# Optimization experiments

Hardware: AMD Instinct MI355X
Metric: run time of the kernel (lower is better)

The kernel has to match this reference:

```python
import jax, jax.numpy as jnp
import numpy as np

MIN_VAL = 0.0
MAX_VAL = 1.0
NUM_BINS = 512
NUM_NODES = 128
GRAD_SMOOTH = 0.01
BIN_W = (MAX_VAL - MIN_VAL) / NUM_BINS


def _make_kernels():
    sobel = jnp.array([-1.0, 0.0, 1.0], dtype=jnp.float32) / (2.0 * BIN_W)
    r = max(1, int(GRAD_SMOOTH / BIN_W))  # kernel radius in bins
    idx = jnp.arange(2 * r + 1, dtype=jnp.float32) - r
    sigma = GRAD_SMOOTH / BIN_W
    g = jnp.exp(-0.5 * (idx / sigma) ** 2)
    return sobel, g / jnp.sum(g)


def _conv1d_reflect(x, k):
    # x: [N, B], k: [K]; torch Conv1d = cross-correlation with reflect padding
    pad = (k.shape[0] - 1) // 2
    xp = jnp.pad(x, ((0, 0), (pad, pad)), mode='reflect')
    out = jax.lax.conv_general_dilated(
        xp[:, None, :], k[None, None, :], (1,), 'VALID',
        dimension_numbers=('NCH', 'OIH', 'NCH'))
    return out[:, 0, :]


def _compute_cdf_pdf(residuals, weights, src_indices, dst_indices):
    # histogram bin per sample (floor)
    bi = jnp.floor((residuals - MIN_VAL) / BIN_W).astype(jnp.int32)
    valid = (bi >= 0) & (bi < NUM_BINS)
    bi = jnp.clip(bi, 0, NUM_BINS - 1)
    wc = (weights * valid).reshape(-1)  # [N_pairs*K]

    src_comb = (src_indices[:, None] * NUM_BINS + bi).reshape(-1)
    dst_comb = (dst_indices[:, None] * NUM_BINS + bi).reshape(-1)
    nseg = NUM_NODES * NUM_BINS
    hist = (jax.ops.segment_sum(wc, src_comb, num_segments=nseg)
            + jax.ops.segment_sum(wc, dst_comb, num_segments=nseg))
    hist = hist.reshape(NUM_NODES, NUM_BINS)

    wflat = weights.reshape(-1)
    src_exp = jnp.broadcast_to(src_indices[:, None], residuals.shape).reshape(-1)
    dst_exp = jnp.broadcast_to(dst_indices[:, None], residuals.shape).reshape(-1)
    tw = (jax.ops.segment_sum(wflat, src_exp, num_segments=NUM_NODES)
          + jax.ops.segment_sum(wflat, dst_exp, num_segments=NUM_NODES))

    pmf = hist / (tw[:, None] + 1e-10)
    cdf = jnp.cumsum(pmf, axis=1)
    sobel, gauss = _make_kernels()
    pdf = _conv1d_reflect(_conv1d_reflect(cdf, sobel), gauss)
    return cdf, pdf


def _lookup(residuals, weights, cdf, pdf, src_indices, dst_indices):
    # rounded bin for lookup (floor of x + 0.5)
    bi = jnp.floor((residuals - MIN_VAL) / BIN_W + 0.5).astype(jnp.int32)
    valid = (bi >= 0) & (bi < NUM_BINS) & (weights > 0.0)
    bi = jnp.clip(bi, 0, NUM_BINS - 1)
    src_cdf = cdf[src_indices[:, None], bi]
    dst_cdf = cdf[dst_indices[:, None], bi]
    src_grad = pdf[src_indices[:, None], bi] * weights
    dst_grad = pdf[dst_indices[:, None], bi] * weights
    two = jnp.float32(2.0)
    return (jnp.where(valid, src_cdf, two),
            jnp.where(valid, src_grad, 0.0),
            jnp.where(valid, dst_cdf, two),
            jnp.where(valid, dst_grad, 0.0))


def setup_inputs() -> dict:
    key = jax.random.key(0)
    k1, k2, k3, k4 = jax.random.split(key, 4)
    N_pairs, K = 1024, 16384
    return {
        'residuals': jax.random.uniform(k1, (N_pairs, K), dtype=jnp.float32),
        'weights': jax.random.uniform(k2, (N_pairs, K), dtype=jnp.float32),
        'src_indices': jax.random.randint(k3, (N_pairs,), 0, NUM_NODES),
        'dst_indices': jax.random.randint(k4, (N_pairs,), 0, NUM_NODES),
    }


def reference(residuals, weights, src_indices, dst_indices):
    cdf, pdf = _compute_cdf_pdf(residuals, weights, src_indices, dst_indices)
    src_cdf, _, dst_cdf, _ = _lookup(residuals, weights, cdf, pdf,
                                     src_indices, dst_indices)
    return src_cdf, dst_cdf
```

## Files before the change

### kernel.cpp

```cpp
#include <hip/hip_runtime.h>

#define NUM_BINS  512
#define NUM_NODES 128
#define K_ELEMS   16384
#define N_PAIRS   1024
#define NCOPY     16

typedef float f32x4 __attribute__((ext_vector_type(4)));
typedef float f32x2 __attribute__((ext_vector_type(2)));
typedef unsigned int   u32;
typedef unsigned short u16;

__device__ __forceinline__ void gfadd(float* p, float v) { unsafeAtomicAdd(p, v); }

__global__ __launch_bounds__(256) void zero_ws_kernel(float* __restrict__ ws, int n)
{
    int i = blockIdx.x * 256 + threadIdx.x;
    if (i < n) ws[i] = 0.0f;
}

__global__ __launch_bounds__(512) void hist_kernel(
    const float* __restrict__ residuals, const float* __restrict__ weights,
    const int* __restrict__ src, const int* __restrict__ dst,
    float* __restrict__ hist, float* __restrict__ tw,
    u32* __restrict__ mask)
{
    __shared__ u32 lh[NUM_BINS * NCOPY];
    __shared__ float swsum[8];
    const int row  = blockIdx.x;
    const int t    = threadIdx.x;
    const int copy = t & 15;

    uint4* lh4 = (uint4*)lh;
    #pragma unroll
    for (int k = 0; k < NUM_BINS * NCOPY / 4 / 512; ++k) {
        uint4 z; z.x = z.y = z.z = z.w = 0u;
        lh4[t + k * 512] = z;
    }
    __syncthreads();

    const f32x4* r4 = (const f32x4*)(residuals + (size_t)row * K_ELEMS);
    const f32x4* w4 = (const f32x4*)(weights   + (size_t)row * K_ELEMS);

    float wsum = 0.0f;
    u32 vbits = 0;

    f32x4 rA = r4[t];
    f32x4 wA = __builtin_nontemporal_load(w4 + t);
    #pragma unroll
    for (int it = 0; it < K_ELEMS / 4 / 512; ++it) {
        f32x4 rB, wB;
        if (it < K_ELEMS / 4 / 512 - 1) {
            rB = r4[t + (it + 1) * 512];
            wB = __builtin_nontemporal_load(w4 + (t + (it + 1) * 512));
        }
        wsum += wA[0] + wA[1] + wA[2] + wA[3];
        #pragma unroll
        for (int c = 0; c < 4; ++c) {
            int b = (int)floorf(rA[c] * 512.0f);
            if ((unsigned)b < 512u)
                atomicAdd(&lh[b * NCOPY + copy], (u32)fmaf(wA[c], 65536.0f, 0.5f));
            int lb = (int)floorf(rA[c] * 512.0f + 0.5f);
            if (((unsigned)lb < 512u) & (wA[c] > 0.0f))
                vbits |= 1u << (it * 4 + c);
        }
        rA = rB; wA = wB;
    }
    mask[(size_t)row * 512 + t] = vbits;

    #pragma unroll
    for (int off = 32; off > 0; off >>= 1) wsum += __shfl_down(wsum, off, 64);
    const int wave = t >> 6, lane = t & 63;
    if (lane == 0) swsum[wave] = wsum;
    __syncthreads();

    const int s = src[row], d = dst[row];
    if (t == 0) {
        float tot = 0.0f;
        #pragma unroll
        for (int i = 0; i < 8; ++i) tot += swsum[i];
        gfadd(&tw[s], tot);
        gfadd(&tw[d], tot);
    }

    {
        u32 tot = 0;
        #pragma unroll
        for (int cc = 0; cc < NCOPY; ++cc)
            tot += lh[t * NCOPY + ((t + cc) & 15)];
        float v = (float)tot * (1.0f / 65536.0f);
        gfadd(&hist[s * NUM_BINS + t], v);
        gfadd(&hist[d * NUM_BINS + t], v);
    }
}

__global__ __launch_bounds__(512) void lookup_scan_kernel(
    const float* __restrict__ residuals, const u32* __restrict__ mask,
    const int* __restrict__ src, const int* __restrict__ dst,
    const float* __restrict__ hist, const float* __restrict__ tw,
    float* __restrict__ out_src, float* __restrict__ out_dst)
{
    __shared__ f32x2 sd[NUM_BINS];
    const int row = blockIdx.x;
    const int t   = threadIdx.x;

    const size_t base = (size_t)row * K_ELEMS;
    const f32x4* r4   = (const f32x4*)(residuals + base);

    f32x4 rr0 = r4[t],           rr1 = r4[t + 512];
    f32x4 rr2 = r4[t + 1024],    rr3 = r4[t + 1536];
    f32x4 rr4 = r4[t + 2048],    rr5 = r4[t + 2560];
    f32x4 rr6 = r4[t + 3072],    rr7 = r4[t + 3584];
    const u32 mw = mask[(size_t)row * 512 + t];

    const int s = src[row], d = dst[row];
    {
        f32x2 v;
        v[0] = hist[s * NUM_BINS + t] / (tw[s] + 1e-10f);
        v[1] = hist[d * NUM_BINS + t] / (tw[d] + 1e-10f);
        sd[t] = v;
    }
    __syncthreads();

    for (int off = 1; off < NUM_BINS; off <<= 1) {
        f32x2 add = (t >= off) ? sd[t - off] : (f32x2){0.0f, 0.0f};
        __syncthreads();
        sd[t] += add;
        __syncthreads();
    }

    f32x4* os4 = (f32x4*)(out_src + base);
    f32x4* od4 = (f32x4*)(out_dst + base);

    #define EMIT(IT, RV)                                                       \
    {                                                                          \
        f32x4 osv, odv;                                                        \
        _Pragma("unroll")                                                      \
        for (int c = 0; c < 4; ++c) {                                          \
            int lb = (int)floorf(RV[c] * 512.0f + 0.5f);                       \
            int bc = min(max(lb, 0), NUM_BINS - 1);                            \
            bool v = (mw >> (IT * 4 + c)) & 1u;                                \
            f32x2 vv = v ? sd[bc] : (f32x2){2.0f, 2.0f};                       \
            osv[c] = vv[0]; odv[c] = vv[1];                                    \
        }                                                                      \
        __builtin_nontemporal_store(osv, os4 + (t + IT * 512));                \
        __builtin_nontemporal_store(odv, od4 + (t + IT * 512));                \
    }
    EMIT(0, rr0) EMIT(1, rr1) EMIT(2, rr2) EMIT(3, rr3)
    EMIT(4, rr4) EMIT(5, rr5) EMIT(6, rr6) EMIT(7, rr7)
    #undef EMIT
}

extern "C" void kernel_launch(void* const* d_in, const int* in_sizes, int n_in,
                              void* d_out, int out_size, void* d_ws, size_t ws_size,
                              hipStream_t stream)
{
    const float* residuals = (const float*)d_in[0];
    const float* weights   = (const float*)d_in[1];
    const int*   src       = (const int*)d_in[2];
    const int*   dst       = (const int*)d_in[3];

    float* out_src = (float*)d_out;
    float* out_dst = out_src + (size_t)N_PAIRS * K_ELEMS;

    float* hist = (float*)d_ws;
    float* tw   = hist + NUM_NODES * NUM_BINS;
    u32*   mask = (u32*)((char*)d_ws + (4u << 20));

    const int ws_elems = NUM_NODES * NUM_BINS + NUM_NODES;
    zero_ws_kernel<<<(ws_elems + 255) / 256, 256, 0, stream>>>((float*)d_ws, ws_elems);

    hist_kernel<<<N_PAIRS, 512, 0, stream>>>(residuals, weights, src, dst,
                                             hist, tw, mask);

    lookup_scan_kernel<<<N_PAIRS, 512, 0, stream>>>(residuals, mask, src, dst,
                                                    hist, tw, out_src, out_dst);
}
```

Measured before the change: 64.32 us.

## Replace global atomic node histograms with per-row histograms gathered in lookup kernel

The histogram kernel now writes each row's integer histogram and weight sum to its own workspace slot, replacing the float atomics into per-node bins. This removes the zeroing kernel and global atomic contention. Each lookup block instead builds a list of the rows that share its src/dst node and sums their histograms and weight sums itself. That adds roughly 2×16 row reads per block, mostly served from L2, and caps the list at 320 rows, which would silently drop rows if one node had more. Summing in integers also makes the accumulation order deterministic.

```diff
diff --git a/kernel.cpp b/kernel.cpp
--- a/kernel.cpp
+++ b/kernel.cpp
@@ -5,24 +5,16 @@
 #define K_ELEMS   16384
 #define N_PAIRS   1024
 #define NCOPY     16
+#define LIST_MAX  320
 
 typedef float f32x4 __attribute__((ext_vector_type(4)));
 typedef float f32x2 __attribute__((ext_vector_type(2)));
 typedef unsigned int   u32;
 typedef unsigned short u16;
 
-__device__ __forceinline__ void gfadd(float* p, float v) { unsafeAtomicAdd(p, v); }
-
-__global__ __launch_bounds__(256) void zero_ws_kernel(float* __restrict__ ws, int n)
-{
-    int i = blockIdx.x * 256 + threadIdx.x;
-    if (i < n) ws[i] = 0.0f;
-}
-
 __global__ __launch_bounds__(512) void hist_kernel(
     const float* __restrict__ residuals, const float* __restrict__ weights,
-    const int* __restrict__ src, const int* __restrict__ dst,
-    float* __restrict__ hist, float* __restrict__ tw,
+    u32* __restrict__ rowhist, float* __restrict__ rowwsum,
     u32* __restrict__ mask)
 {
     __shared__ u32 lh[NUM_BINS * NCOPY];
@@ -74,13 +66,11 @@
     if (lane == 0) swsum[wave] = wsum;
     __syncthreads();
 
-    const int s = src[row], d = dst[row];
     if (t == 0) {
         float tot = 0.0f;
         #pragma unroll
         for (int i = 0; i < 8; ++i) tot += swsum[i];
-        gfadd(&tw[s], tot);
-        gfadd(&tw[d], tot);
+        rowwsum[row] = tot;
     }
 
     {
@@ -88,36 +78,97 @@
         #pragma unroll
         for (int cc = 0; cc < NCOPY; ++cc)
             tot += lh[t * NCOPY + ((t + cc) & 15)];
-        float v = (float)tot * (1.0f / 65536.0f);
-        gfadd(&hist[s * NUM_BINS + t], v);
-        gfadd(&hist[d * NUM_BINS + t], v);
+        rowhist[(size_t)row * NUM_BINS + t] = tot;
     }
 }
 
 __global__ __launch_bounds__(512) void lookup_scan_kernel(
     const float* __restrict__ residuals, const u32* __restrict__ mask,
     const int* __restrict__ src, const int* __restrict__ dst,
-    const float* __restrict__ hist, const float* __restrict__ tw,
+    const u32* __restrict__ rowhist, const float* __restrict__ rowwsum,
     float* __restrict__ out_src, float* __restrict__ out_dst)
 {
     __shared__ f32x2 sd[NUM_BINS];
+    __shared__ int   ssrc[N_PAIRS];
+    __shared__ int   sdst[N_PAIRS];
+    __shared__ float rw[N_PAIRS];
+    __shared__ u16   listS[LIST_MAX], listD[LIST_MAX];
+    __shared__ u32   cntS, cntD;
+    __shared__ float twsh[16];
+
     const int row = blockIdx.x;
     const int t   = threadIdx.x;
 
     const size_t base = (size_t)row * K_ELEMS;
     const f32x4* r4   = (const f32x4*)(residuals + base);
 
-    f32x4 rr0 = r4[t],           rr1 = r4[t + 512];
-    f32x4 rr2 = r4[t + 1024],    rr3 = r4[t + 1536];
-    f32x4 rr4 = r4[t + 2048],    rr5 = r4[t + 2560];
-    f32x4 rr6 = r4[t + 3072],    rr7 = r4[t + 3584];
+    f32x4 rr0 = r4[t],        rr1 = r4[t + 512];
+    f32x4 rr2 = r4[t + 1024], rr3 = r4[t + 1536];
+    f32x4 rr4 = r4[t + 2048], rr5 = r4[t + 2560];
+    f32x4 rr6 = r4[t + 3072], rr7 = r4[t + 3584];
     const u32 mw = mask[(size_t)row * 512 + t];
 
-    const int s = src[row], d = dst[row];
+    if (t == 0) { cntS = 0; cntD = 0; }
+    ssrc[t] = src[t];  ssrc[t + 512] = src[t + 512];
+    sdst[t] = dst[t];  sdst[t + 512] = dst[t + 512];
+    rw[t] = rowwsum[t]; rw[t + 512] = rowwsum[t + 512];
+    __syncthreads();
+
+    const int s = ssrc[row], d = sdst[row];
+
+    float pS = 0.0f, pD = 0.0f;
+    #pragma unroll
+    for (int h = 0; h < 2; ++h) {
+        const int r = t + h * 512;
+        const int rs = ssrc[r], rd = sdst[r];
+        const float w = rw[r];
+        if (rs == s) { u32 i = atomicAdd(&cntS, 1u); if (i < LIST_MAX) listS[i] = (u16)r; pS += w; }
+        if (rd == s) { u32 i = atomicAdd(&cntS, 1u); if (i < LIST_MAX) listS[i] = (u16)r; pS += w; }
+        if (rs == d) { u32 i = atomicAdd(&cntD, 1u); if (i < LIST_MAX) listD[i] = (u16)r; pD += w; }
+        if (rd == d) { u32 i = atomicAdd(&cntD, 1u); if (i < LIST_MAX) listD[i] = (u16)r; pD += w; }
+    }
+    #pragma unroll
+    for (int off = 32; off > 0; off >>= 1) {
+        pS += __shfl_down(pS, off, 64);
+        pD += __shfl_down(pD, off, 64);
+    }
+    if ((t & 63) == 0) { twsh[(t >> 6) * 2] = pS; twsh[(t >> 6) * 2 + 1] = pD; }
+    __syncthreads();
+
+    float twS = 0.0f, twD = 0.0f;
+    #pragma unroll
+    for (int i = 0; i < 8; ++i) { twS += twsh[i * 2]; twD += twsh[i * 2 + 1]; }
+
+    const int nS = (int)min(cntS, (u32)LIST_MAX);
+    const int nD = (int)min(cntD, (u32)LIST_MAX);
+    u32 accS = 0, accD = 0;
+    {
+        int i = 0;
+        for (; i + 4 <= nS; i += 4) {
+            u32 a0 = rowhist[(size_t)listS[i]     * NUM_BINS + t];
+            u32 a1 = rowhist[(size_t)listS[i + 1] * NUM_BINS + t];
+            u32 a2 = rowhist[(size_t)listS[i + 2] * NUM_BINS + t];
+            u32 a3 = rowhist[(size_t)listS[i + 3] * NUM_BINS + t];
+            accS += a0 + a1 + a2 + a3;
+        }
+        for (; i < nS; ++i) accS += rowhist[(size_t)listS[i] * NUM_BINS + t];
+    }
+    {
+        int i = 0;
+        for (; i + 4 <= nD; i += 4) {
+            u32 a0 = rowhist[(size_t)listD[i]     * NUM_BINS + t];
+            u32 a1 = rowhist[(size_t)listD[i + 1] * NUM_BINS + t];
+            u32 a2 = rowhist[(size_t)listD[i + 2] * NUM_BINS + t];
+            u32 a3 = rowhist[(size_t)listD[i + 3] * NUM_BINS + t];
+            accD += a0 + a1 + a2 + a3;
+        }
+        for (; i < nD; ++i) accD += rowhist[(size_t)listD[i] * NUM_BINS + t];
+    }
+
     {
         f32x2 v;
-        v[0] = hist[s * NUM_BINS + t] / (tw[s] + 1e-10f);
-        v[1] = hist[d * NUM_BINS + t] / (tw[d] + 1e-10f);
+        v[0] = (float)accS * (1.0f / 65536.0f) / (twS + 1e-10f);
+        v[1] = (float)accD * (1.0f / 65536.0f) / (twD + 1e-10f);
         sd[t] = v;
     }
     __syncthreads();
@@ -163,16 +214,14 @@
     float* out_src = (float*)d_out;
     float* out_dst = out_src + (size_t)N_PAIRS * K_ELEMS;
 
-    float* hist = (float*)d_ws;
-    float* tw   = hist + NUM_NODES * NUM_BINS;
-    u32*   mask = (u32*)((char*)d_ws + (4u << 20));
-
-    const int ws_elems = NUM_NODES * NUM_BINS + NUM_NODES;
-    zero_ws_kernel<<<(ws_elems + 255) / 256, 256, 0, stream>>>((float*)d_ws, ws_elems);
-
-    hist_kernel<<<N_PAIRS, 512, 0, stream>>>(residuals, weights, src, dst,
-                                             hist, tw, mask);
+    u32*   rowhist = (u32*)d_ws;
+    float* rowwsum = (float*)((char*)d_ws + (2u << 20));
+    u32*   mask    = (u32*)((char*)d_ws + (4u << 20));
+
+    hist_kernel<<<N_PAIRS, 512, 0, stream>>>(residuals, weights,
+                                             rowhist, rowwsum, mask);
 
     lookup_scan_kernel<<<N_PAIRS, 512, 0, stream>>>(residuals, mask, src, dst,
-                                                    hist, tw, out_src, out_dst);
+                                                    rowhist, rowwsum,
+                                                    out_src, out_dst);
 }
```

Result: slower. 66.31 us (+3.1%).
